# Optimization experiments

Hardware: AMD Instinct MI355X
Metric: run time of the kernel (lower is better)

The kernel has to match this reference:

```python
import jax, jax.numpy as jnp
import numpy as np

B, S_ENC, S_DEC, ENC_H, DEC_H = 8, 2048, 2048, 512, 512


def setup_inputs() -> dict:
    key = jax.random.key(0)
    k1, k2, k3 = jax.random.split(key, 3)
    return {
        "enc_hidden_states": jax.random.normal(k1, (B, S_ENC, ENC_H), dtype=jnp.float32),
        "dec_hidden_states": jax.random.normal(k2, (B, S_DEC, DEC_H), dtype=jnp.float32),
        "W_att": jax.random.normal(k3, (ENC_H, DEC_H), dtype=jnp.float32),
    }


def reference(enc_hidden_states, dec_hidden_states, W_att):
    # Project encoder states: [B, S_enc, dec_h]
    enc_proj = jnp.einsum("bse,ed->bsd", enc_hidden_states, W_att)
    # Luong 'general' scores for all decoder timesteps at once: [B, S_dec, S_enc]
    # (original code loops over decoder timesteps via tf.map_fn; this is the
    # equivalent single batched matmul)
    att_logits = jnp.einsum("btd,bsd->bts", dec_hidden_states, enc_proj)
    att_softmax = jax.nn.softmax(att_logits, axis=-1)
    # Attention context vectors: [B, S_dec, enc_h]
    att_vector = jnp.einsum("bts,bse->bte", att_softmax, enc_hidden_states)
    return att_vector
```

## Files before the change

kernel.cpp:

```cpp
#include <hip/hip_runtime.h>
#include <cstdint>


#define DEVINL __device__ __forceinline__

typedef __attribute__((ext_vector_type(8))) short short8;
typedef __attribute__((ext_vector_type(4))) float f32x4;

DEVINL short f2bf(float x) {
    union { float f; uint32_t u; } v; v.f = x;
    uint32_t r = v.u + 0x7FFFu + ((v.u >> 16) & 1u);
    return (short)(r >> 16);
}
DEVINL float bf2f(short h) {
    union { uint32_t u; float f; } v; v.u = ((uint32_t)(uint16_t)h) << 16;
    return v.f;
}

DEVINL void gload_lds16(const void* g, void* l) {
    __builtin_amdgcn_global_load_lds(
        (const __attribute__((address_space(1))) char*)g,
        (__attribute__((address_space(3))) char*)l, 16, 0, 0);
}

__global__ __launch_bounds__(256)
void split_kernel(const float* __restrict__ x, short* __restrict__ hi,
                  short* __restrict__ lo)
{
    long i = ((long)blockIdx.x * 256 + threadIdx.x) * 8;
    f32x4 a = *(const f32x4*)(x + i);
    f32x4 b = *(const f32x4*)(x + i + 4);
    short8 h, l;
#pragma unroll
    for (int j = 0; j < 4; j++) {
        short ha = f2bf(a[j]); h[j] = ha;     l[j] = f2bf(a[j] - bf2f(ha));
        short hb = f2bf(b[j]); h[4 + j] = hb; l[4 + j] = f2bf(b[j] - bf2f(hb));
    }
    *(short8*)(hi + i) = h;
    *(short8*)(lo + i) = l;
}

__global__ __launch_bounds__(256)
void split_w_kernel(const float* __restrict__ w, short* __restrict__ wth,
                    short* __restrict__ wtl)
{
    int idx = blockIdx.x * 256 + threadIdx.x;
    int k = idx >> 9, n = idx & 511;
    float v = w[idx];
    short h = f2bf(v);
    wth[(long)n * 512 + k] = h;
    wtl[(long)n * 512 + k] = f2bf(v - bf2f(h));
}

__global__ __launch_bounds__(256)
void transpose_bf16_kernel(const float* __restrict__ x, short* __restrict__ xt)
{
    __shared__ short tile[32][33];
    const int b  = blockIdx.z;
    const int s0 = blockIdx.x * 32;
    const int e0 = blockIdx.y * 32;
    const float* px = x + (long)b * 2048 * 512;
    short* pt = xt + (long)b * 512 * 2048;
    const int tx = threadIdx.x & 31;
    const int ty = threadIdx.x >> 5;
#pragma unroll
    for (int r = 0; r < 32; r += 8)
        tile[ty + r][tx] = f2bf(px[(long)(s0 + ty + r) * 512 + e0 + tx]);
    __syncthreads();
#pragma unroll
    for (int r = 0; r < 32; r += 8)
        pt[(long)(e0 + ty + r) * 2048 + s0 + tx] = tile[tx][ty + r];
}

template<int NTERMS, bool SPLIT_OUT>
__global__ __launch_bounds__(256, 2)
void gemm_bt(const short* __restrict__ Ah, const short* __restrict__ Al,
             const short* __restrict__ Bh, const short* __restrict__ Bl,
             float* __restrict__ C, short* __restrict__ Ch, short* __restrict__ Cl,
             int K, int lda, int ldb, int ldc,
             long sA, long sB, long sC)
{
    extern __shared__ char smem_raw[];
    constexpr int OPS = (NTERMS == 3) ? 4 : 2;
    constexpr int SET = 128 * 32 * OPS;
    short* smem = (short*)smem_raw;

    const int tid  = threadIdx.x;
    const int wave = tid >> 6;
    const int lane = tid & 63;
    const int quad = lane >> 4;
    const int l16  = lane & 15;
    const int wm   = (wave >> 1) * 64;
    const int wn   = (wave & 1) * 64;

    const long tile_m = (long)blockIdx.y * 128;
    const long tile_n = (long)blockIdx.x * 128;
    const int  bz     = blockIdx.z;

    const short* pAh = Ah + (long)bz * sA;
    const short* pBh = Bh + (long)bz * sB;
    const short* pAl = (NTERMS == 3) ? (Al + (long)bz * sA) : nullptr;
    const short* pBl = (NTERMS == 3) ? (Bl + (long)bz * sB) : nullptr;

    const int srow = tid >> 2;
    const int skq  = (tid & 3) * 8;
    const int lds_off = srow * 32 + skq;
    const long ga0 = (tile_m + srow) * (long)lda + skq;
    const long gb0 = (tile_n + srow) * (long)ldb + skq;

    auto stage = [&](int k0, int buf) {
        short* s   = smem + buf * SET;
        short* ash = s;
        short* bsh = s + 128 * 32;
        gload_lds16(pAh + ga0 + k0,             ash + lds_off);
        gload_lds16(pAh + ga0 + 64l * lda + k0, ash + lds_off + 64 * 32);
        gload_lds16(pBh + gb0 + k0,             bsh + lds_off);
        gload_lds16(pBh + gb0 + 64l * ldb + k0, bsh + lds_off + 64 * 32);
        if constexpr (NTERMS == 3) {
            short* asl = s + 2 * 128 * 32;
            short* bsl = s + 3 * 128 * 32;
            gload_lds16(pAl + ga0 + k0,             asl + lds_off);
            gload_lds16(pAl + ga0 + 64l * lda + k0, asl + lds_off + 64 * 32);
            gload_lds16(pBl + gb0 + k0,             bsl + lds_off);
            gload_lds16(pBl + gb0 + 64l * ldb + k0, bsl + lds_off + 64 * 32);
        }
    };

    f32x4 acc[4][4] = {};
    stage(0, 0);
    int cur = 0;

    for (int k0 = 0; k0 < K; k0 += 32) {
        __syncthreads();
        if (k0 + 32 < K) stage(k0 + 32, cur ^ 1);

        short* s   = smem + cur * SET;
        short* ash = s;
        short* bsh = s + 128 * 32;
        short* asl = s + 2 * 128 * 32;
        short* bsl = s + 3 * 128 * 32;

        short8 ah[4], bh[4], al[4], bl[4];
#pragma unroll
        for (int i = 0; i < 4; i++) {
            ah[i] = *(const short8*)&ash[(wm + i * 16 + l16) * 32 + quad * 8];
            bh[i] = *(const short8*)&bsh[(wn + i * 16 + l16) * 32 + quad * 8];
            if constexpr (NTERMS == 3) {
                al[i] = *(const short8*)&asl[(wm + i * 16 + l16) * 32 + quad * 8];
                bl[i] = *(const short8*)&bsl[(wn + i * 16 + l16) * 32 + quad * 8];
            }
        }
#pragma unroll
        for (int i = 0; i < 4; i++)
#pragma unroll
            for (int j = 0; j < 4; j++) {
                acc[i][j] = __builtin_amdgcn_mfma_f32_16x16x32_bf16(ah[i], bh[j], acc[i][j], 0, 0, 0);
                if constexpr (NTERMS == 3) {
                    acc[i][j] = __builtin_amdgcn_mfma_f32_16x16x32_bf16(ah[i], bl[j], acc[i][j], 0, 0, 0);
                    acc[i][j] = __builtin_amdgcn_mfma_f32_16x16x32_bf16(al[i], bh[j], acc[i][j], 0, 0, 0);
                }
            }
        cur ^= 1;
    }

#pragma unroll
    for (int i = 0; i < 4; i++)
#pragma unroll
        for (int j = 0; j < 4; j++) {
            const long row0 = tile_m + wm + i * 16 + quad * 4;
            const long col  = tile_n + wn + j * 16 + l16;
#pragma unroll
            for (int r = 0; r < 4; r++) {
                float v = acc[i][j][r];
                if constexpr (SPLIT_OUT) {
                    long idx = (long)bz * sC + (row0 + r) * (long)ldc + col;
                    short h = f2bf(v);
                    Ch[idx] = h;
                    Cl[idx] = f2bf(v - bf2f(h));
                } else {
                    C[(long)bz * sC + (row0 + r) * (long)ldc + col] = v;
                }
            }
        }
}

__global__ __launch_bounds__(512, 2)
void gemm3_256(const short* __restrict__ Ah, const short* __restrict__ Al,
               const short* __restrict__ Bh, const short* __restrict__ Bl,
               float* __restrict__ C,
               int K, int lda, int ldb, int ldc,
               long sA, long sB, long sC, int nbx, int nby)
{
    extern __shared__ char smem_raw[];
    short* smem = (short*)smem_raw;
    constexpr int PL  = 256 * 32;
    constexpr int SET = 4 * PL;

    const int t    = threadIdx.x;
    const int wave = t >> 6;
    const int lane = t & 63;
    const int quad = lane >> 4;
    const int l16  = lane & 15;
    const int wm   = (wave >> 2) * 128;
    const int wn   = (wave & 3) * 64;
    const int kslot8 = ((quad ^ ((l16 >> 1) & 3)) << 3);

    const int nwg = gridDim.x;
    const int wg  = blockIdx.x;
    const int swz = (wg & 7) * (nwg >> 3) + (wg >> 3);
    const int per_b = nbx * nby;
    const int bz  = swz / per_b;
    const int rem = swz - bz * per_b;
    const long tile_m = (long)(rem / nbx) * 256;
    const long tile_n = (long)(rem % nbx) * 256;

    const short* pAh = Ah + (long)bz * sA;
    const short* pAl = Al + (long)bz * sA;
    const short* pBh = Bh + (long)bz * sB;
    const short* pBl = Bl + (long)bz * sB;

    const int srow   = t >> 2;
    const int schunk = (t & 3) ^ ((t >> 3) & 3);
    const long gA  = (tile_m + srow) * (long)lda + schunk * 8;
    const long gB  = (tile_n + srow) * (long)ldb + schunk * 8;
    const long gA2 = gA + 128l * lda;
    const long gB2 = gB + 128l * ldb;
    const int ld0 = t * 8;

    f32x4 acc[8][4] = {};

    {
        short* s = smem;
        gload_lds16(pAh + gA,  s + ld0);
        gload_lds16(pAh + gA2, s + ld0 + 4096);
        gload_lds16(pBh + gB,  s + 2 * PL + ld0);
        gload_lds16(pBh + gB2, s + 2 * PL + ld0 + 4096);
        gload_lds16(pAl + gA,  s + PL + ld0);
        gload_lds16(pAl + gA2, s + PL + ld0 + 4096);
        gload_lds16(pBl + gB,  s + 3 * PL + ld0);
        gload_lds16(pBl + gB2, s + 3 * PL + ld0 + 4096);
    }
    asm volatile("s_waitcnt vmcnt(0)" ::: "memory");
    __builtin_amdgcn_s_barrier();

    const int NT = K >> 5;
    int cur = 0;
#pragma unroll 1
    for (int kt = 0; kt < NT; ++kt) {
        const short* s    = smem + cur * SET;
        short* sn         = smem + (cur ^ 1) * SET;
        const short* ah_p = s;
        const short* al_p = s + PL;
        const short* bh_p = s + 2 * PL;
        const short* bl_p = s + 3 * PL;
        const int  k0n  = (kt + 1) << 5;
        const bool more = (kt + 1 < NT);

        short8 xah[8], xbh[4], xal[4], xbl[4];

#pragma unroll
        for (int i = 0; i < 4; i++)
            xah[i] = *(const short8*)&ah_p[(wm + i * 16 + l16) * 32 + kslot8];
#pragma unroll
        for (int j = 0; j < 4; j++)
            xbh[j] = *(const short8*)&bh_p[(wn + j * 16 + l16) * 32 + kslot8];
        if (more) {
            gload_lds16(pAh + gA  + k0n, sn + ld0);
            gload_lds16(pAh + gA2 + k0n, sn + ld0 + 4096);
        }
        __builtin_amdgcn_s_barrier();
        asm volatile("s_waitcnt lgkmcnt(0)" ::: "memory");
        __builtin_amdgcn_sched_barrier(0);
        __builtin_amdgcn_s_setprio(1);
#pragma unroll
        for (int i = 0; i < 4; i++)
#pragma unroll
            for (int j = 0; j < 4; j++)
                acc[i][j] = __builtin_amdgcn_mfma_f32_16x16x32_bf16(xah[i], xbh[j], acc[i][j], 0, 0, 0);
        __builtin_amdgcn_s_setprio(0);
        __builtin_amdgcn_s_barrier();

#pragma unroll
        for (int i = 4; i < 8; i++)
            xah[i] = *(const short8*)&ah_p[(wm + i * 16 + l16) * 32 + kslot8];
        if (more) {
            gload_lds16(pBh + gB  + k0n, sn + 2 * PL + ld0);
            gload_lds16(pBh + gB2 + k0n, sn + 2 * PL + ld0 + 4096);
        }
        __builtin_amdgcn_s_barrier();
        asm volatile("s_waitcnt lgkmcnt(0)" ::: "memory");
        __builtin_amdgcn_sched_barrier(0);
        __builtin_amdgcn_s_setprio(1);
#pragma unroll
        for (int i = 4; i < 8; i++)
#pragma unroll
            for (int j = 0; j < 4; j++)
                acc[i][j] = __builtin_amdgcn_mfma_f32_16x16x32_bf16(xah[i], xbh[j], acc[i][j], 0, 0, 0);
        __builtin_amdgcn_s_setprio(0);
        __builtin_amdgcn_s_barrier();

#pragma unroll
        for (int i = 0; i < 4; i++)
            xal[i] = *(const short8*)&al_p[(wm + i * 16 + l16) * 32 + kslot8];
        if (more) {
            gload_lds16(pAl + gA  + k0n, sn + PL + ld0);
            gload_lds16(pAl + gA2 + k0n, sn + PL + ld0 + 4096);
        }
        __builtin_amdgcn_s_barrier();
        asm volatile("s_waitcnt lgkmcnt(0)" ::: "memory");
        __builtin_amdgcn_sched_barrier(0);
        __builtin_amdgcn_s_setprio(1);
#pragma unroll
        for (int i = 0; i < 4; i++)
#pragma unroll
            for (int j = 0; j < 4; j++)
                acc[i][j] = __builtin_amdgcn_mfma_f32_16x16x32_bf16(xal[i], xbh[j], acc[i][j], 0, 0, 0);
        __builtin_amdgcn_s_setprio(0);
        __builtin_amdgcn_s_barrier();

#pragma unroll
        for (int i = 0; i < 4; i++)
            xal[i] = *(const short8*)&al_p[(wm + 64 + i * 16 + l16) * 32 + kslot8];
        if (more) {
            gload_lds16(pBl + gB  + k0n, sn + 3 * PL + ld0);
            gload_lds16(pBl + gB2 + k0n, sn + 3 * PL + ld0 + 4096);
        }
        __builtin_amdgcn_s_barrier();
        asm volatile("s_waitcnt lgkmcnt(0)" ::: "memory");
        __builtin_amdgcn_sched_barrier(0);
        __builtin_amdgcn_s_setprio(1);
#pragma unroll
        for (int i = 0; i < 4; i++)
#pragma unroll
            for (int j = 0; j < 4; j++)
                acc[4 + i][j] = __builtin_amdgcn_mfma_f32_16x16x32_bf16(xal[i], xbh[j], acc[4 + i][j], 0, 0, 0);
        __builtin_amdgcn_s_setprio(0);
        __builtin_amdgcn_s_barrier();

#pragma unroll
        for (int j = 0; j < 4; j++)
            xbl[j] = *(const short8*)&bl_p[(wn + j * 16 + l16) * 32 + kslot8];
        __builtin_amdgcn_s_barrier();
        asm volatile("s_waitcnt lgkmcnt(0)" ::: "memory");
        __builtin_amdgcn_sched_barrier(0);
        __builtin_amdgcn_s_setprio(1);
#pragma unroll
        for (int i = 0; i < 4; i++)
#pragma unroll
            for (int j = 0; j < 4; j++)
                acc[i][j] = __builtin_amdgcn_mfma_f32_16x16x32_bf16(xah[i], xbl[j], acc[i][j], 0, 0, 0);
        __builtin_amdgcn_s_setprio(0);
        __builtin_amdgcn_s_barrier();

        __builtin_amdgcn_s_setprio(1);
#pragma unroll
        for (int i = 4; i < 8; i++)
#pragma unroll
            for (int j = 0; j < 4; j++)
                acc[i][j] = __builtin_amdgcn_mfma_f32_16x16x32_bf16(xah[i], xbl[j], acc[i][j], 0, 0, 0);
        __builtin_amdgcn_s_setprio(0);
        asm volatile("s_waitcnt vmcnt(0)" ::: "memory");
        __builtin_amdgcn_s_barrier();

        cur ^= 1;
    }

#pragma unroll
    for (int i = 0; i < 8; i++)
#pragma unroll
        for (int j = 0; j < 4; j++) {
            const long row0 = tile_m + wm + i * 16 + quad * 4;
            const long col  = tile_n + wn + j * 16 + l16;
#pragma unroll
            for (int r = 0; r < 4; r++)
                C[(long)bz * sC + (row0 + r) * (long)ldc + col] = acc[i][j][r];
        }
}

__global__ __launch_bounds__(256)
void softmax_kernel(const float* __restrict__ logits, short* __restrict__ P)
{
    const long row = blockIdx.x;
    const float* p = logits + row * 2048;
    const int tid = threadIdx.x;
    const int lane = tid & 63, wave = tid >> 6;

    f32x4 v0 = *(const f32x4*)(p + tid * 8);
    f32x4 v1 = *(const f32x4*)(p + tid * 8 + 4);

    float m = fmaxf(fmaxf(fmaxf(v0[0], v0[1]), fmaxf(v0[2], v0[3])),
                    fmaxf(fmaxf(v1[0], v1[1]), fmaxf(v1[2], v1[3])));
#pragma unroll
    for (int o = 32; o > 0; o >>= 1) m = fmaxf(m, __shfl_xor(m, o));

    __shared__ float red[8];
    if (lane == 0) red[wave] = m;
    __syncthreads();
    m = fmaxf(fmaxf(red[0], red[1]), fmaxf(red[2], red[3]));

    float e[8];
    float s = 0.f;
#pragma unroll
    for (int i = 0; i < 4; i++) { e[i] = __expf(v0[i] - m); s += e[i]; }
#pragma unroll
    for (int i = 0; i < 4; i++) { e[4 + i] = __expf(v1[i] - m); s += e[4 + i]; }
#pragma unroll
    for (int o = 32; o > 0; o >>= 1) s += __shfl_xor(s, o);
    if (lane == 0) red[4 + wave] = s;
    __syncthreads();
    const float inv = 1.f / (red[4] + red[5] + red[6] + red[7]);

    short8 ob;
#pragma unroll
    for (int i = 0; i < 8; i++) ob[i] = f2bf(e[i] * inv);
    *(short8*)(P + row * 2048 + tid * 8) = ob;
}

extern "C" void kernel_launch(void* const* d_in, const int* in_sizes, int n_in,
                              void* d_out, int out_size, void* d_ws, size_t ws_size,
                              hipStream_t stream)
{
    const float* enc = (const float*)d_in[0];
    const float* dec = (const float*)d_in[1];
    const float* W   = (const float*)d_in[2];
    float* out = (float*)d_out;

    const long BSE = 8l * 2048 * 512;
    const long NW  = 512l * 512;

    char* p = (char*)d_ws;
    auto take = [&](long bytes) { char* r = p; p += (bytes + 255) & ~255l; return r; };
    short* enc_hi = (short*)take(BSE * 2);
    short* enc_lo = (short*)take(BSE * 2);
    short* dec_hi = (short*)take(BSE * 2);
    short* dec_lo = (short*)take(BSE * 2);
    short* ep_hi  = (short*)take(BSE * 2);
    short* ep_lo  = (short*)take(BSE * 2);
    short* enc_t  = (short*)take(BSE * 2);
    short* wt_hi  = (short*)take(NW * 2);
    short* wt_lo  = (short*)take(NW * 2);
    float* logits = (float*)take(8l * 2048 * 2048 * 4);
    short* Pbuf = enc_hi;
    (void)ws_size; (void)in_sizes; (void)n_in; (void)out_size;

    static bool attr_set = false;
    if (!attr_set) {
        (void)hipFuncSetAttribute((const void*)gemm3_256,
                                  hipFuncAttributeMaxDynamicSharedMemorySize,
                                  131072);
        attr_set = true;
    }

    split_kernel<<<4096, 256, 0, stream>>>(enc, enc_hi, enc_lo);
    split_kernel<<<4096, 256, 0, stream>>>(dec, dec_hi, dec_lo);
    split_w_kernel<<<1024, 256, 0, stream>>>(W, wt_hi, wt_lo);
    transpose_bf16_kernel<<<dim3(64, 16, 8), 256, 0, stream>>>(enc, enc_t);

    gemm_bt<3, true><<<dim3(4, 128, 1), 256, 64 * 1024, stream>>>(
        enc_hi, enc_lo, wt_hi, wt_lo, nullptr, ep_hi, ep_lo,
        512, 512, 512, 512, 0, 0, 0);

    gemm3_256<<<512, 512, 131072, stream>>>(
        dec_hi, dec_lo, ep_hi, ep_lo, logits,
        512, 512, 512, 2048, 2048l * 512, 2048l * 512, 2048l * 2048, 8, 8);

    softmax_kernel<<<16384, 256, 0, stream>>>(logits, Pbuf);

    gemm_bt<1, false><<<dim3(4, 16, 8), 256, 32 * 1024, stream>>>(
        Pbuf, nullptr, enc_t, nullptr, out, nullptr, nullptr,
        2048, 2048, 2048, 512, 2048l * 2048, 512l * 2048, 2048l * 512);
}
```

Baseline: 353.9 us.

## Load B operand directly into registers in logits GEMM and fuse enc split with transpose

The 256x256 three-term logits GEMM now loads its B operand (hi and lo parts of the projected encoder) straight from global memory into registers, double-buffered across a two-tile unrolled loop, instead of staging it through LDS. This halves the LDS footprint per block, which could allow more blocks per CU, and removes the LDS reads for B. The encoder hi/lo split is also fused into the transpose kernel, so the encoder is read once and one launch is dropped. The tradeoffs are more VGPR use, uncoalesced per-lane global loads for B, and a changed wait/barrier schedule.

```diff
diff --git a/kernel.cpp b/kernel.cpp
--- a/kernel.cpp
+++ b/kernel.cpp
@@ -53,19 +53,28 @@
 }
 
 __global__ __launch_bounds__(256)
-void transpose_bf16_kernel(const float* __restrict__ x, short* __restrict__ xt)
+void split_transpose_kernel(const float* __restrict__ x, short* __restrict__ hi,
+                            short* __restrict__ lo, short* __restrict__ xt)
 {
     __shared__ short tile[32][33];
     const int b  = blockIdx.z;
     const int s0 = blockIdx.x * 32;
     const int e0 = blockIdx.y * 32;
     const float* px = x + (long)b * 2048 * 512;
+    short* ph = hi + (long)b * 2048 * 512;
+    short* pl = lo + (long)b * 2048 * 512;
     short* pt = xt + (long)b * 512 * 2048;
     const int tx = threadIdx.x & 31;
     const int ty = threadIdx.x >> 5;
 #pragma unroll
-    for (int r = 0; r < 32; r += 8)
-        tile[ty + r][tx] = f2bf(px[(long)(s0 + ty + r) * 512 + e0 + tx]);
+    for (int r = 0; r < 32; r += 8) {
+        long idx = (long)(s0 + ty + r) * 512 + e0 + tx;
+        float v = px[idx];
+        short h = f2bf(v);
+        ph[idx] = h;
+        pl[idx] = f2bf(v - bf2f(h));
+        tile[ty + r][tx] = h;
+    }
     __syncthreads();
 #pragma unroll
     for (int r = 0; r < 32; r += 8)
@@ -194,7 +203,7 @@
     extern __shared__ char smem_raw[];
     short* smem = (short*)smem_raw;
     constexpr int PL  = 256 * 32;
-    constexpr int SET = 4 * PL;
+    constexpr int SET = 2 * PL;
 
     const int t    = threadIdx.x;
     const int wave = t >> 6;
@@ -222,51 +231,48 @@
     const int srow   = t >> 2;
     const int schunk = (t & 3) ^ ((t >> 3) & 3);
     const long gA  = (tile_m + srow) * (long)lda + schunk * 8;
-    const long gB  = (tile_n + srow) * (long)ldb + schunk * 8;
     const long gA2 = gA + 128l * lda;
-    const long gB2 = gB + 128l * ldb;
     const int ld0 = t * 8;
 
+    int gb[4];
+#pragma unroll
+    for (int j = 0; j < 4; j++)
+        gb[j] = (int)((tile_n + wn + j * 16 + l16) * (long)ldb + quad * 8);
+
     f32x4 acc[8][4] = {};
+    short8 bh0[4], bh1[4], blc[4];
 
     {
         short* s = smem;
         gload_lds16(pAh + gA,  s + ld0);
         gload_lds16(pAh + gA2, s + ld0 + 4096);
-        gload_lds16(pBh + gB,  s + 2 * PL + ld0);
-        gload_lds16(pBh + gB2, s + 2 * PL + ld0 + 4096);
         gload_lds16(pAl + gA,  s + PL + ld0);
         gload_lds16(pAl + gA2, s + PL + ld0 + 4096);
-        gload_lds16(pBl + gB,  s + 3 * PL + ld0);
-        gload_lds16(pBl + gB2, s + 3 * PL + ld0 + 4096);
-    }
+    }
+#pragma unroll
+    for (int j = 0; j < 4; j++) bh0[j] = *(const short8*)(pBh + gb[j]);
+#pragma unroll
+    for (int j = 0; j < 4; j++) blc[j] = *(const short8*)(pBl + gb[j]);
     asm volatile("s_waitcnt vmcnt(0)" ::: "memory");
     __builtin_amdgcn_s_barrier();
 
-    const int NT = K >> 5;
-    int cur = 0;
-#pragma unroll 1
-    for (int kt = 0; kt < NT; ++kt) {
-        const short* s    = smem + cur * SET;
+    auto run_tile = [&](int cur, short8 (&bhU)[4], short8 (&bhF)[4],
+                        int k0n, bool more) {
+        const short* sp   = smem + cur * SET;
         short* sn         = smem + (cur ^ 1) * SET;
-        const short* ah_p = s;
-        const short* al_p = s + PL;
-        const short* bh_p = s + 2 * PL;
-        const short* bl_p = s + 3 * PL;
-        const int  k0n  = (kt + 1) << 5;
-        const bool more = (kt + 1 < NT);
-
-        short8 xah[8], xbh[4], xal[4], xbl[4];
+        const short* ah_p = sp;
+        const short* al_p = sp + PL;
+        short8 xah[8], xal[4];
 
 #pragma unroll
         for (int i = 0; i < 4; i++)
             xah[i] = *(const short8*)&ah_p[(wm + i * 16 + l16) * 32 + kslot8];
-#pragma unroll
-        for (int j = 0; j < 4; j++)
-            xbh[j] = *(const short8*)&bh_p[(wn + j * 16 + l16) * 32 + kslot8];
         if (more) {
             gload_lds16(pAh + gA  + k0n, sn + ld0);
             gload_lds16(pAh + gA2 + k0n, sn + ld0 + 4096);
+#pragma unroll
+            for (int j = 0; j < 4; j++)
+                bhF[j] = *(const short8*)(pBh + gb[j] + k0n);
         }
         __builtin_amdgcn_s_barrier();
         asm volatile("s_waitcnt lgkmcnt(0)" ::: "memory");
@@ -276,36 +282,45 @@
         for (int i = 0; i < 4; i++)
 #pragma unroll
             for (int j = 0; j < 4; j++)
-                acc[i][j] = __builtin_amdgcn_mfma_f32_16x16x32_bf16(xah[i], xbh[j], acc[i][j], 0, 0, 0);
+                acc[i][j] = __builtin_amdgcn_mfma_f32_16x16x32_bf16(xah[i], bhU[j], acc[i][j], 0, 0, 0);
         __builtin_amdgcn_s_setprio(0);
         __builtin_amdgcn_s_barrier();
 
 #pragma unroll
-        for (int i = 4; i < 8; i++)
-            xah[i] = *(const short8*)&ah_p[(wm + i * 16 + l16) * 32 + kslot8];
+        for (int i = 0; i < 4; i++)
+            xah[4 + i] = *(const short8*)&ah_p[(wm + 64 + i * 16 + l16) * 32 + kslot8];
         if (more) {
-            gload_lds16(pBh + gB  + k0n, sn + 2 * PL + ld0);
-            gload_lds16(pBh + gB2 + k0n, sn + 2 * PL + ld0 + 4096);
+            gload_lds16(pAl + gA  + k0n, sn + PL + ld0);
+            gload_lds16(pAl + gA2 + k0n, sn + PL + ld0 + 4096);
         }
         __builtin_amdgcn_s_barrier();
         asm volatile("s_waitcnt lgkmcnt(0)" ::: "memory");
         __builtin_amdgcn_sched_barrier(0);
         __builtin_amdgcn_s_setprio(1);
 #pragma unroll
-        for (int i = 4; i < 8; i++)
-#pragma unroll
-            for (int j = 0; j < 4; j++)
-                acc[i][j] = __builtin_amdgcn_mfma_f32_16x16x32_bf16(xah[i], xbh[j], acc[i][j], 0, 0, 0);
+        for (int i = 0; i < 4; i++)
+#pragma unroll
+            for (int j = 0; j < 4; j++)
+                acc[4 + i][j] = __builtin_amdgcn_mfma_f32_16x16x32_bf16(xah[4 + i], bhU[j], acc[4 + i][j], 0, 0, 0);
         __builtin_amdgcn_s_setprio(0);
         __builtin_amdgcn_s_barrier();
 
+        __builtin_amdgcn_s_setprio(1);
+#pragma unroll
+        for (int i = 0; i < 8; i++)
+#pragma unroll
+            for (int j = 0; j < 4; j++)
+                acc[i][j] = __builtin_amdgcn_mfma_f32_16x16x32_bf16(xah[i], blc[j], acc[i][j], 0, 0, 0);
+        __builtin_amdgcn_s_setprio(0);
+        if (more) {
+#pragma unroll
+            for (int j = 0; j < 4; j++)
+                blc[j] = *(const short8*)(pBl + gb[j] + k0n);
+        }
+
 #pragma unroll
         for (int i = 0; i < 4; i++)
             xal[i] = *(const short8*)&al_p[(wm + i * 16 + l16) * 32 + kslot8];
-        if (more) {
-            gload_lds16(pAl + gA  + k0n, sn + PL + ld0);
-            gload_lds16(pAl + gA2 + k0n, sn + PL + ld0 + 4096);
-        }
         __builtin_amdgcn_s_barrier();
         asm volatile("s_waitcnt lgkmcnt(0)" ::: "memory");
         __builtin_amdgcn_sched_barrier(0);
@@ -314,17 +329,13 @@
         for (int i = 0; i < 4; i++)
 #pragma unroll
             for (int j = 0; j < 4; j++)
-                acc[i][j] = __builtin_amdgcn_mfma_f32_16x16x32_bf16(xal[i], xbh[j], acc[i][j], 0, 0, 0);
+                acc[i][j] = __builtin_amdgcn_mfma_f32_16x16x32_bf16(xal[i], bhU[j], acc[i][j], 0, 0, 0);
         __builtin_amdgcn_s_setprio(0);
         __builtin_amdgcn_s_barrier();
 
 #pragma unroll
         for (int i = 0; i < 4; i++)
             xal[i] = *(const short8*)&al_p[(wm + 64 + i * 16 + l16) * 32 + kslot8];
-        if (more) {
-            gload_lds16(pBl + gB  + k0n, sn + 3 * PL + ld0);
-            gload_lds16(pBl + gB2 + k0n, sn + 3 * PL + ld0 + 4096);
-        }
         __builtin_amdgcn_s_barrier();
         asm volatile("s_waitcnt lgkmcnt(0)" ::: "memory");
         __builtin_amdgcn_sched_barrier(0);
@@ -333,36 +344,18 @@
         for (int i = 0; i < 4; i++)
 #pragma unroll
             for (int j = 0; j < 4; j++)
-                acc[4 + i][j] = __builtin_amdgcn_mfma_f32_16x16x32_bf16(xal[i], xbh[j], acc[4 + i][j], 0, 0, 0);
+                acc[4 + i][j] = __builtin_amdgcn_mfma_f32_16x16x32_bf16(xal[i], bhU[j], acc[4 + i][j], 0, 0, 0);
         __builtin_amdgcn_s_setprio(0);
-        __builtin_amdgcn_s_barrier();
-
-#pragma unroll
-        for (int j = 0; j < 4; j++)
-            xbl[j] = *(const short8*)&bl_p[(wn + j * 16 + l16) * 32 + kslot8];
-        __builtin_amdgcn_s_barrier();
-        asm volatile("s_waitcnt lgkmcnt(0)" ::: "memory");
-        __builtin_amdgcn_sched_barrier(0);
-        __builtin_amdgcn_s_setprio(1);
-#pragma unroll
-        for (int i = 0; i < 4; i++)
-#pragma unroll
-            for (int j = 0; j < 4; j++)
-                acc[i][j] = __builtin_amdgcn_mfma_f32_16x16x32_bf16(xah[i], xbl[j], acc[i][j], 0, 0, 0);
-        __builtin_amdgcn_s_setprio(0);
-        __builtin_amdgcn_s_barrier();
-
-        __builtin_amdgcn_s_setprio(1);
-#pragma unroll
-        for (int i = 4; i < 8; i++)
-#pragma unroll
-            for (int j = 0; j < 4; j++)
-                acc[i][j] = __builtin_amdgcn_mfma_f32_16x16x32_bf16(xah[i], xbl[j], acc[i][j], 0, 0, 0);
-        __builtin_amdgcn_s_setprio(0);
-        asm volatile("s_waitcnt vmcnt(0)" ::: "memory");
-        __builtin_amdgcn_s_barrier();
-
-        cur ^= 1;
+        if (more)
+            asm volatile("s_waitcnt vmcnt(4)" ::: "memory");
+        __builtin_amdgcn_s_barrier();
+    };
+
+    const int NT = K >> 5;
+#pragma unroll 1
+    for (int kt = 0; kt < NT; kt += 2) {
+        run_tile(0, bh0, bh1, (kt + 1) << 5, kt + 1 < NT);
+        run_tile(1, bh1, bh0, (kt + 2) << 5, kt + 2 < NT);
     }
 
 #pragma unroll
@@ -447,20 +440,20 @@
     if (!attr_set) {
         (void)hipFuncSetAttribute((const void*)gemm3_256,
                                   hipFuncAttributeMaxDynamicSharedMemorySize,
-                                  131072);
+                                  65536);
         attr_set = true;
     }
 
-    split_kernel<<<4096, 256, 0, stream>>>(enc, enc_hi, enc_lo);
+    split_transpose_kernel<<<dim3(64, 16, 8), 256, 0, stream>>>(
+        enc, enc_hi, enc_lo, enc_t);
     split_kernel<<<4096, 256, 0, stream>>>(dec, dec_hi, dec_lo);
     split_w_kernel<<<1024, 256, 0, stream>>>(W, wt_hi, wt_lo);
-    transpose_bf16_kernel<<<dim3(64, 16, 8), 256, 0, stream>>>(enc, enc_t);
 
     gemm_bt<3, true><<<dim3(4, 128, 1), 256, 64 * 1024, stream>>>(
         enc_hi, enc_lo, wt_hi, wt_lo, nullptr, ep_hi, ep_lo,
         512, 512, 512, 512, 0, 0, 0);
 
-    gemm3_256<<<512, 512, 131072, stream>>>(
+    gemm3_256<<<512, 512, 65536, stream>>>(
         dec_hi, dec_lo, ep_hi, ep_lo, logits,
         512, 512, 512, 2048, 2048l * 512, 2048l * 512, 2048l * 2048, 8, 8);
 
```

Result: slower. 480.9 us (+35.9%).

## Fuse encoder split with transpose and restructure 3-term GEMM LDS/MFMA schedule

Applied to the files above, without the earlier changes.

The encoder split and the bf16 transpose kernels are merged into one kernel, so the fp32 encoder tensor is read once and one launch goes away. The 3-term GEMM main loop is reordered. All hi fragments of A and B, plus the B-lo fragments, are loaded up front. The A-lo loads are interleaved between MFMA blocks, and several intermediate barriers and explicit lgkmcnt waits are removed, so LDS reads overlap MFMA work. The cost is higher register pressure from holding more fragments at once. Removing the lgkmcnt waits relies on compiler-inserted waits for correctness.

```diff
diff --git a/kernel.cpp b/kernel.cpp
--- a/kernel.cpp
+++ b/kernel.cpp
@@ -53,19 +53,28 @@
 }
 
 __global__ __launch_bounds__(256)
-void transpose_bf16_kernel(const float* __restrict__ x, short* __restrict__ xt)
+void split_transpose_kernel(const float* __restrict__ x, short* __restrict__ hi,
+                            short* __restrict__ lo, short* __restrict__ xt)
 {
     __shared__ short tile[32][33];
     const int b  = blockIdx.z;
     const int s0 = blockIdx.x * 32;
     const int e0 = blockIdx.y * 32;
     const float* px = x + (long)b * 2048 * 512;
+    short* ph = hi + (long)b * 2048 * 512;
+    short* pl = lo + (long)b * 2048 * 512;
     short* pt = xt + (long)b * 512 * 2048;
     const int tx = threadIdx.x & 31;
     const int ty = threadIdx.x >> 5;
 #pragma unroll
-    for (int r = 0; r < 32; r += 8)
-        tile[ty + r][tx] = f2bf(px[(long)(s0 + ty + r) * 512 + e0 + tx]);
+    for (int r = 0; r < 32; r += 8) {
+        long idx = (long)(s0 + ty + r) * 512 + e0 + tx;
+        float v = px[idx];
+        short h = f2bf(v);
+        ph[idx] = h;
+        pl[idx] = f2bf(v - bf2f(h));
+        tile[ty + r][tx] = h;
+    }
     __syncthreads();
 #pragma unroll
     for (int r = 0; r < 32; r += 8)
@@ -256,110 +265,99 @@
         const int  k0n  = (kt + 1) << 5;
         const bool more = (kt + 1 < NT);
 
-        short8 xah[8], xbh[4], xal[4], xbl[4];
-
-#pragma unroll
-        for (int i = 0; i < 4; i++)
-            xah[i] = *(const short8*)&ah_p[(wm + i * 16 + l16) * 32 + kslot8];
+        short8 ahA[4], ahB[4], xbh[4], xbl[4], alA[4], alB[4];
+
+#pragma unroll
+        for (int i = 0; i < 4; i++)
+            ahA[i] = *(const short8*)&ah_p[(wm + i * 16 + l16) * 32 + kslot8];
 #pragma unroll
         for (int j = 0; j < 4; j++)
             xbh[j] = *(const short8*)&bh_p[(wn + j * 16 + l16) * 32 + kslot8];
+        __builtin_amdgcn_sched_barrier(0);
+
+#pragma unroll
+        for (int i = 0; i < 4; i++)
+            ahB[i] = *(const short8*)&ah_p[(wm + 64 + i * 16 + l16) * 32 + kslot8];
+#pragma unroll
+        for (int j = 0; j < 4; j++)
+            xbl[j] = *(const short8*)&bl_p[(wn + j * 16 + l16) * 32 + kslot8];
         if (more) {
             gload_lds16(pAh + gA  + k0n, sn + ld0);
             gload_lds16(pAh + gA2 + k0n, sn + ld0 + 4096);
         }
-        __builtin_amdgcn_s_barrier();
-        asm volatile("s_waitcnt lgkmcnt(0)" ::: "memory");
         __builtin_amdgcn_sched_barrier(0);
+        __builtin_amdgcn_s_barrier();
         __builtin_amdgcn_s_setprio(1);
 #pragma unroll
         for (int i = 0; i < 4; i++)
 #pragma unroll
             for (int j = 0; j < 4; j++)
-                acc[i][j] = __builtin_amdgcn_mfma_f32_16x16x32_bf16(xah[i], xbh[j], acc[i][j], 0, 0, 0);
+                acc[i][j] = __builtin_amdgcn_mfma_f32_16x16x32_bf16(ahA[i], xbh[j], acc[i][j], 0, 0, 0);
         __builtin_amdgcn_s_setprio(0);
-        __builtin_amdgcn_s_barrier();
-
-#pragma unroll
-        for (int i = 4; i < 8; i++)
-            xah[i] = *(const short8*)&ah_p[(wm + i * 16 + l16) * 32 + kslot8];
+
+#pragma unroll
+        for (int i = 0; i < 4; i++)
+            alA[i] = *(const short8*)&al_p[(wm + i * 16 + l16) * 32 + kslot8];
         if (more) {
             gload_lds16(pBh + gB  + k0n, sn + 2 * PL + ld0);
             gload_lds16(pBh + gB2 + k0n, sn + 2 * PL + ld0 + 4096);
         }
-        __builtin_amdgcn_s_barrier();
-        asm volatile("s_waitcnt lgkmcnt(0)" ::: "memory");
         __builtin_amdgcn_sched_barrier(0);
+        __builtin_amdgcn_s_barrier();
         __builtin_amdgcn_s_setprio(1);
 #pragma unroll
-        for (int i = 4; i < 8; i++)
-#pragma unroll
-            for (int j = 0; j < 4; j++)
-                acc[i][j] = __builtin_amdgcn_mfma_f32_16x16x32_bf16(xah[i], xbh[j], acc[i][j], 0, 0, 0);
+        for (int i = 0; i < 4; i++)
+#pragma unroll
+            for (int j = 0; j < 4; j++)
+                acc[4 + i][j] = __builtin_amdgcn_mfma_f32_16x16x32_bf16(ahB[i], xbh[j], acc[4 + i][j], 0, 0, 0);
         __builtin_amdgcn_s_setprio(0);
-        __builtin_amdgcn_s_barrier();
-
-#pragma unroll
-        for (int i = 0; i < 4; i++)
-            xal[i] = *(const short8*)&al_p[(wm + i * 16 + l16) * 32 + kslot8];
+
+#pragma unroll
+        for (int i = 0; i < 4; i++)
+            alB[i] = *(const short8*)&al_p[(wm + 64 + i * 16 + l16) * 32 + kslot8];
         if (more) {
             gload_lds16(pAl + gA  + k0n, sn + PL + ld0);
             gload_lds16(pAl + gA2 + k0n, sn + PL + ld0 + 4096);
         }
-        __builtin_amdgcn_s_barrier();
-        asm volatile("s_waitcnt lgkmcnt(0)" ::: "memory");
         __builtin_amdgcn_sched_barrier(0);
+        __builtin_amdgcn_s_barrier();
         __builtin_amdgcn_s_setprio(1);
 #pragma unroll
         for (int i = 0; i < 4; i++)
 #pragma unroll
             for (int j = 0; j < 4; j++)
-                acc[i][j] = __builtin_amdgcn_mfma_f32_16x16x32_bf16(xal[i], xbh[j], acc[i][j], 0, 0, 0);
+                acc[i][j] = __builtin_amdgcn_mfma_f32_16x16x32_bf16(ahA[i], xbl[j], acc[i][j], 0, 0, 0);
         __builtin_amdgcn_s_setprio(0);
-        __builtin_amdgcn_s_barrier();
-
-#pragma unroll
-        for (int i = 0; i < 4; i++)
-            xal[i] = *(const short8*)&al_p[(wm + 64 + i * 16 + l16) * 32 + kslot8];
+
         if (more) {
             gload_lds16(pBl + gB  + k0n, sn + 3 * PL + ld0);
             gload_lds16(pBl + gB2 + k0n, sn + 3 * PL + ld0 + 4096);
         }
-        __builtin_amdgcn_s_barrier();
-        asm volatile("s_waitcnt lgkmcnt(0)" ::: "memory");
         __builtin_amdgcn_sched_barrier(0);
+        __builtin_amdgcn_s_barrier();
         __builtin_amdgcn_s_setprio(1);
 #pragma unroll
         for (int i = 0; i < 4; i++)
 #pragma unroll
             for (int j = 0; j < 4; j++)
-                acc[4 + i][j] = __builtin_amdgcn_mfma_f32_16x16x32_bf16(xal[i], xbh[j], acc[4 + i][j], 0, 0, 0);
+                acc[4 + i][j] = __builtin_amdgcn_mfma_f32_16x16x32_bf16(ahB[i], xbl[j], acc[4 + i][j], 0, 0, 0);
         __builtin_amdgcn_s_setprio(0);
         __builtin_amdgcn_s_barrier();
 
-#pragma unroll
-        for (int j = 0; j < 4; j++)
-            xbl[j] = *(const short8*)&bl_p[(wn + j * 16 + l16) * 32 + kslot8];
-        __builtin_amdgcn_s_barrier();
-        asm volatile("s_waitcnt lgkmcnt(0)" ::: "memory");
-        __builtin_amdgcn_sched_barrier(0);
         __builtin_amdgcn_s_setprio(1);
 #pragma unroll
         for (int i = 0; i < 4; i++)
 #pragma unroll
             for (int j = 0; j < 4; j++)
-                acc[i][j] = __builtin_amdgcn_mfma_f32_16x16x32_bf16(xah[i], xbl[j], acc[i][j], 0, 0, 0);
+                acc[i][j] = __builtin_amdgcn_mfma_f32_16x16x32_bf16(alA[i], xbh[j], acc[i][j], 0, 0, 0);
+#pragma unroll
+        for (int i = 0; i < 4; i++)
+#pragma unroll
+            for (int j = 0; j < 4; j++)
+                acc[4 + i][j] = __builtin_amdgcn_mfma_f32_16x16x32_bf16(alB[i], xbh[j], acc[4 + i][j], 0, 0, 0);
         __builtin_amdgcn_s_setprio(0);
-        __builtin_amdgcn_s_barrier();
-
-        __builtin_amdgcn_s_setprio(1);
-#pragma unroll
-        for (int i = 4; i < 8; i++)
-#pragma unroll
-            for (int j = 0; j < 4; j++)
-                acc[i][j] = __builtin_amdgcn_mfma_f32_16x16x32_bf16(xah[i], xbl[j], acc[i][j], 0, 0, 0);
-        __builtin_amdgcn_s_setprio(0);
-        asm volatile("s_waitcnt vmcnt(0)" ::: "memory");
+        if (more)
+            asm volatile("s_waitcnt vmcnt(0)" ::: "memory");
         __builtin_amdgcn_s_barrier();
 
         cur ^= 1;
@@ -451,10 +449,10 @@
         attr_set = true;
     }
 
-    split_kernel<<<4096, 256, 0, stream>>>(enc, enc_hi, enc_lo);
+    split_transpose_kernel<<<dim3(64, 16, 8), 256, 0, stream>>>(
+        enc, enc_hi, enc_lo, enc_t);
     split_kernel<<<4096, 256, 0, stream>>>(dec, dec_hi, dec_lo);
     split_w_kernel<<<1024, 256, 0, stream>>>(W, wt_hi, wt_lo);
-    transpose_bf16_kernel<<<dim3(64, 16, 8), 256, 0, stream>>>(enc, enc_t);
 
     gemm_bt<3, true><<<dim3(4, 128, 1), 256, 64 * 1024, stream>>>(
         enc_hi, enc_lo, wt_hi, wt_lo, nullptr, ep_hi, ep_lo,
```

Result: faster. 335.2 us (-5.3%).
